# Kernel tuning notes

Measured on AMD Instinct MI355X. Metric: run time of the kernel, lower is better.

The kernel has to match this reference:

```python
import jax, jax.numpy as jnp
import numpy as np

B, N1, R12, R23 = 1, 4096, 4, 4
N2, N3 = N1 * R12, N1 * R12 * R23
D, F, H, NCLS, K = 1024, 512, 256, 4, 256


def setup_inputs() -> dict:
    key = jax.random.key(0)
    ks = jax.random.split(key, 10)
    s = 0.02
    return {
        "x1": jax.random.normal(ks[0], (B, N1, D), jnp.float32),
        "x2": jax.random.normal(ks[1], (B, N2, D), jnp.float32),
        "x3": jax.random.normal(ks[2], (B, N3, D), jnp.float32),
        # 3 fc layers (low/mid/high mag): Linear(D->F)
        "fcW": (jax.random.normal(ks[3], (3, D, F), jnp.float32) * s),
        "fcb": jnp.zeros((3, F), jnp.float32),
        # 5 gated-attention modules: 0=ga_low,1=ga_mid,2=ga_high,3=aux_low,4=aux_mid
        "gaWa": (jax.random.normal(ks[4], (5, F, H), jnp.float32) * s),
        "gaba": jnp.zeros((5, H), jnp.float32),
        "gaWb": (jax.random.normal(ks[5], (5, F, H), jnp.float32) * s),
        "gabb": jnp.zeros((5, H), jnp.float32),
        "gaWc": (jax.random.normal(ks[6], (5, H, 1), jnp.float32) * s),
        "gabc": jnp.zeros((5, 1), jnp.float32),
        "Wh": (jax.random.normal(ks[7], (F, NCLS), jnp.float32) * s),
        "bh": jnp.zeros((NCLS,), jnp.float32),
        "k_sample": K,
    }


def _ga(x, i, Wa, ba, Wb, bb, Wc, bc):
    # GatedAttention: tanh branch * sigmoid branch -> Linear(H->1); returns (B,N)
    a = jnp.tanh(x @ Wa[i] + ba[i])
    g = jax.nn.sigmoid(x @ Wb[i] + bb[i])
    return ((a * g) @ Wc[i] + bc[i])[..., 0]


def _block_gather(x, idx, ratio):
    # Equivalent to einsum('bkn,bnd->bkd', kron(one_hot(idx), eye(ratio)), x):
    # pick contiguous blocks of `ratio` rows for each selected coarse index.
    b, n, d = x.shape
    xb = x.reshape(b, n // ratio, ratio, d)
    out = jnp.take_along_axis(xb, idx[:, :, None, None], axis=1)  # (B,k,ratio,D)
    return out.reshape(b, idx.shape[1] * ratio, d)


def reference(x1, x2, x3, fcW, fcb, gaWa, gaba, gaWb, gabb, gaWc, gabc, Wh, bh, k_sample):
    ga = (gaWa, gaba, gaWb, gabb, gaWc, gabc)
    n1, n2, n3 = x1.shape[1], x2.shape[1], x3.shape[1]

    # --- low mag ---
    h1 = jax.nn.relu(x1 @ fcW[0] + fcb[0])                    # (B,N1,F)
    A1 = jax.nn.softmax(_ga(h1, 0, *ga), axis=-1)             # (B,N1)
    M1 = jnp.einsum('bn,bnf->bf', A1, h1)                     # (B,F)
    A1_aux = jax.nn.softmax(_ga(h1, 3, *ga), axis=-1)
    k1 = min(n1, int(k_sample))
    idx1 = jnp.sort(jax.lax.top_k(A1_aux, k1)[1], axis=-1)    # (B,k1)

    # zoom: gather selected blocks from mid and high mag features
    x2s = _block_gather(x2, idx1, n2 // n1)                   # (B,k1*R12,D)
    x3s = _block_gather(x3, idx1, n3 // n1)                   # (B,k1*R12*R23,D)

    # --- mid mag ---
    h2 = jax.nn.relu(x2s @ fcW[1] + fcb[1])
    A2 = jax.nn.softmax(_ga(h2, 1, *ga), axis=-1)
    M2 = jnp.einsum('bn,bnf->bf', A2, h2)
    A2_aux = jax.nn.softmax(_ga(h2, 4, *ga), axis=-1)
    k2 = min(h2.shape[1], int(k_sample))
    idx2 = jnp.sort(jax.lax.top_k(A2_aux, k2)[1], axis=-1)

    x3s2 = _block_gather(x3s, idx2, n3 // n2)                 # (B,k2*R23,D)

    # --- high mag ---
    h3 = jax.nn.relu(x3s2 @ fcW[2] + fcb[2])
    A3 = jax.nn.softmax(_ga(h3, 2, *ga), axis=-1)
    M3 = jnp.einsum('bn,bnf->bf', A3, h3)

    M = M1 + M2 + M3                                           # (B,F)
    logits = M @ Wh + bh                                       # (B,NCLS)
    return logits
```

## Files before the change

kernel.cpp:

```cpp
#include <hip/hip_runtime.h>
#include <hip/hip_bf16.h>
#include <math.h>


typedef __attribute__((ext_vector_type(8))) short short8;
typedef __attribute__((ext_vector_type(4))) float float4a;

__device__ __forceinline__ ushort f2bf(float f) {
    unsigned u = __float_as_uint(f);
    return (ushort)((u + 0x7fffu + ((u >> 16) & 1u)) >> 16);
}
__device__ __forceinline__ uint pk2(float a, float b) {
    __hip_bfloat162 t = __float22bfloat162_rn(make_float2(a, b));
    uint u; __builtin_memcpy(&u, &t, 4); return u;
}
__device__ __forceinline__ float aload(const float* p) {
    return __hip_atomic_load(p, __ATOMIC_RELAXED, __HIP_MEMORY_SCOPE_AGENT);
}

template<int SPLIT>
__global__ __launch_bounds__(256) void zm_hgemm(
    const float* __restrict__ A, int lda,
    const int* __restrict__ rowmap,
    const ushort* __restrict__ Bt,
    const float* __restrict__ bias,
    float* __restrict__ Cf, ushort* __restrict__ Cb, int ldc, int K)
{
    __shared__ ushort As[64 * 40];
    __shared__ ushort Bs[64 * 40];
    const int tid = threadIdx.x;
    const int brow = blockIdx.y << 6;
    const int bcol = blockIdx.x << 6;
    const int kbeg = SPLIT ? ((int)blockIdx.z << 8) : 0;
    const int kend = SPLIT ? kbeg + 256 : K;

    const int sr = tid >> 2;
    const int sk = (tid & 3) << 3;
    int arow = brow + sr;
    if (rowmap) arow = rowmap[arow];
    const float* Ap = A + (size_t)arow * lda;
    const ushort* Bp = Bt + (size_t)(bcol + sr) * K + sk;

    const int w = tid >> 6;
    const int wm = (w >> 1) << 5;
    const int wn = (w & 1) << 5;
    const int lane = tid & 63;
    const int lm = lane & 15;
    const int lq = lane >> 4;

    float4a acc[2][2] = {};

    for (int k0 = kbeg; k0 < kend; k0 += 32) {
        const float* ap = Ap + k0 + sk;
        float4 v0 = *(const float4*)(ap);
        float4 v1 = *(const float4*)(ap + 4);
        uint4 p0;
        p0.x = pk2(v0.x, v0.y); p0.y = pk2(v0.z, v0.w);
        p0.z = pk2(v1.x, v1.y); p0.w = pk2(v1.z, v1.w);
        *(uint4*)&As[sr * 40 + sk] = p0;
        *(uint4*)&Bs[sr * 40 + sk] = *(const uint4*)(Bp + k0);
        __syncthreads();
        short8 afr[2], bfr[2];
#pragma unroll
        for (int mt = 0; mt < 2; mt++)
            afr[mt] = *(const short8*)&As[(wm + mt * 16 + lm) * 40 + lq * 8];
#pragma unroll
        for (int nt = 0; nt < 2; nt++)
            bfr[nt] = *(const short8*)&Bs[(wn + nt * 16 + lm) * 40 + lq * 8];
#pragma unroll
        for (int mt = 0; mt < 2; mt++)
#pragma unroll
            for (int nt = 0; nt < 2; nt++)
                acc[mt][nt] = __builtin_amdgcn_mfma_f32_16x16x32_bf16(
                    afr[mt], bfr[nt], acc[mt][nt], 0, 0, 0);
        __syncthreads();
    }

#pragma unroll
    for (int mt = 0; mt < 2; mt++) {
#pragma unroll
        for (int nt = 0; nt < 2; nt++) {
            int gc = bcol + wn + nt * 16 + lm;
            float bv = bias[gc];
            if (SPLIT && blockIdx.z != 0) bv = 0.0f;
#pragma unroll
            for (int r = 0; r < 4; r++) {
                int gr = brow + wm + mt * 16 + lq * 4 + r;
                float v = acc[mt][nt][r] + bv;
                if (SPLIT) {
                    atomicAdd(&Cf[(size_t)gr * ldc + gc], v);
                } else {
                    v = fmaxf(v, 0.0f);
                    Cf[(size_t)gr * ldc + gc] = v;
                    Cb[(size_t)gr * ldc + gc] = f2bf(v);
                }
            }
        }
    }
}

template<int AMODE>
__global__ __launch_bounds__(256) void zm_sgemm(
    const void* __restrict__ Av, int lda,
    const ushort* __restrict__ Bt,
    const float* __restrict__ bint,
    const float* __restrict__ wc0, const float* __restrict__ wc1,
    float* __restrict__ sMain, float* __restrict__ sAux,
    float* __restrict__ statsOut, int* __restrict__ cnt2, int lastBlk)
{
    __shared__ ushort As[64 * 40];
    __shared__ ushort Bs[64 * 40];
    __shared__ float part[4][64];
    const int tid = threadIdx.x;
    const int brow = blockIdx.y << 6;
    const int bcol = blockIdx.x << 6;

    const int sr = tid >> 2;
    const int sk = (tid & 3) << 3;
    const float*  Af = (const float*)Av;
    const ushort* Ab = (const ushort*)Av;
    const ushort* Bp = Bt + (size_t)(bcol + sr) * 512 + sk;

    const int w = tid >> 6;
    const int wn = w << 4;
    const int lane = tid & 63;
    const int lm = lane & 15;
    const int lq = lane >> 4;

    float4a acc[4] = {};

    for (int k0 = 0; k0 < 512; k0 += 32) {
        if (AMODE == 0) {
            *(uint4*)&As[sr * 40 + sk] =
                *(const uint4*)(Ab + (size_t)(brow + sr) * lda + k0 + sk);
        } else {
            const float* ap = Af + (size_t)(brow + sr) * lda + k0 + sk;
            float4 v0 = *(const float4*)ap;
            float4 v1 = *(const float4*)(ap + 4);
            v0.x = fmaxf(v0.x, 0.f); v0.y = fmaxf(v0.y, 0.f);
            v0.z = fmaxf(v0.z, 0.f); v0.w = fmaxf(v0.w, 0.f);
            v1.x = fmaxf(v1.x, 0.f); v1.y = fmaxf(v1.y, 0.f);
            v1.z = fmaxf(v1.z, 0.f); v1.w = fmaxf(v1.w, 0.f);
            uint4 pk;
            pk.x = pk2(v0.x, v0.y); pk.y = pk2(v0.z, v0.w);
            pk.z = pk2(v1.x, v1.y); pk.w = pk2(v1.z, v1.w);
            *(uint4*)&As[sr * 40 + sk] = pk;
        }
        *(uint4*)&Bs[sr * 40 + sk] = *(const uint4*)(Bp + k0);
        __syncthreads();
        short8 bfr = *(const short8*)&Bs[(wn + lm) * 40 + lq * 8];
#pragma unroll
        for (int mt = 0; mt < 4; mt++) {
            short8 afr = *(const short8*)&As[(mt * 16 + lm) * 40 + lq * 8];
            acc[mt] = __builtin_amdgcn_mfma_f32_16x16x32_bf16(afr, bfr, acc[mt], 0, 0, 0);
        }
        __syncthreads();
    }

    const int gc = bcol + wn + lm;
    const float* wcp = (gc >= 512) ? wc1 : wc0;
    const float wcv = wcp[(gc & 511) >> 1];
    const float bv = bint[gc];
    const bool odd = (gc & 1);
    float* sp = (bcol >= 512) ? sAux : sMain;

#pragma unroll
    for (int mt = 0; mt < 4; mt++) {
        float red[4];
#pragma unroll
        for (int r = 0; r < 4; r++) {
            float v = acc[mt][r] + bv;
            float x = odd ? (1.0f / (1.0f + expf(-v))) : tanhf(v);
            float prt = __shfl_xor(x, 1);
            float ctr = odd ? 0.0f : (x * prt * wcv);
            ctr += __shfl_xor(ctr, 1);
            ctr += __shfl_xor(ctr, 2);
            ctr += __shfl_xor(ctr, 4);
            ctr += __shfl_xor(ctr, 8);
            red[r] = ctr;
        }
        if (lm == 0) {
#pragma unroll
            for (int r = 0; r < 4; r++) part[w][mt * 16 + lq * 4 + r] = red[r];
        }
    }
    __syncthreads();
    if (tid < 64) {
        float tot = part[0][tid] + part[1][tid] + part[2][tid] + part[3][tid];
        atomicAdd(&sp[brow + tid], tot);
    }

    if (statsOut) {
        __threadfence();
        __shared__ int lastf;
        if (tid == 0)
            lastf = (__hip_atomic_fetch_add(cnt2, 1, __ATOMIC_ACQ_REL,
                                            __HIP_MEMORY_SCOPE_AGENT) == lastBlk);
        __syncthreads();
        if (lastf) {
            float* red = (float*)part;
            float vv[4];
            float mx = -3.4e38f;
#pragma unroll
            for (int j = 0; j < 4; j++) {
                vv[j] = aload(&sMain[tid + j * 256]);
                mx = fmaxf(mx, vv[j]);
            }
            red[tid] = mx; __syncthreads();
            for (int o = 128; o > 0; o >>= 1) {
                if (tid < o) red[tid] = fmaxf(red[tid], red[tid + o]);
                __syncthreads();
            }
            mx = red[0]; __syncthreads();
            float z = 0.0f;
#pragma unroll
            for (int j = 0; j < 4; j++) z += expf(vv[j] - mx);
            red[tid] = z; __syncthreads();
            for (int o = 128; o > 0; o >>= 1) {
                if (tid < o) red[tid] += red[tid + o];
                __syncthreads();
            }
            if (tid == 0) { statsOut[0] = mx; statsOut[1] = red[0]; }
        }
    }
}

__global__ __launch_bounds__(1024) void zm_topk(
    const float* __restrict__ sa, const float* __restrict__ sm, int n,
    const int* __restrict__ idx_prev,
    int* __restrict__ idx_out, int* __restrict__ rm_out,
    float* __restrict__ stOut)
{
    __shared__ float redf[1024];
    __shared__ int hist[256];
    __shared__ int idxbuf[256];
    __shared__ int wsum[16];
    __shared__ int bcastB, bcastAbove;
    const int bs = 1024;
    const int tid = threadIdx.x;

    if (blockIdx.x == 1) {
        float mx = -3.4e38f;
        for (int i = tid; i < n; i += bs) mx = fmaxf(mx, sm[i]);
        redf[tid] = mx; __syncthreads();
        for (int o = 512; o > 0; o >>= 1) {
            if (tid < o) redf[tid] = fmaxf(redf[tid], redf[tid + o]);
            __syncthreads();
        }
        mx = redf[0]; __syncthreads();
        float z = 0.0f;
        for (int i = tid; i < n; i += bs) z += expf(sm[i] - mx);
        redf[tid] = z; __syncthreads();
        for (int o = 512; o > 0; o >>= 1) {
            if (tid < o) redf[tid] += redf[tid + o];
            __syncthreads();
        }
        if (tid == 0) { stOut[0] = mx; stOut[1] = redf[0]; }
        return;
    }

    const int ept = n >> 10;
    const int lane = tid & 63;
    unsigned key[4];
#pragma unroll
    for (int e = 0; e < 4; e++) key[e] = 0;
    for (int e = 0; e < ept; e++) {
        unsigned u = __float_as_uint(sa[tid * ept + e]);
        key[e] = (u & 0x80000000u) ? ~u : (u | 0x80000000u);
    }

    unsigned prefix = 0;
    int remaining = 256;
    for (int pass = 0; pass < 4; pass++) {
        const int shift = 24 - pass * 8;
        if (tid < 256) hist[tid] = 0;
        __syncthreads();
        for (int e = 0; e < ept; e++) {
            unsigned k = key[e];
            bool ok = (pass == 0) || ((k >> (shift + 8)) == (prefix >> (shift + 8)));
            if (ok) atomicAdd(&hist[(k >> shift) & 0xff], 1);
        }
        __syncthreads();
        if (tid < 64) {
            int h0 = hist[lane * 4 + 0], h1 = hist[lane * 4 + 1];
            int h2 = hist[lane * 4 + 2], h3 = hist[lane * 4 + 3];
            int q = h0 + h1 + h2 + h3;
            int suf = q;
#pragma unroll
            for (int o = 1; o < 64; o <<= 1) {
                int v = __shfl_down(suf, o);
                if (lane + o < 64) suf += v;
            }
            int above = suf - q;
            int c3 = above + h3;
            int c2 = c3 + h2;
            int c1 = c2 + h1;
            int c0 = c1 + h0;
            int cc[4]  = {c0, c1, c2, c3};
            int nxt[4] = {c1, c2, c3, above};
#pragma unroll
            for (int j = 0; j < 4; j++)
                if (cc[j] >= remaining && nxt[j] < remaining) {
                    bcastB = lane * 4 + j;
                    bcastAbove = nxt[j];
                }
        }
        __syncthreads();
        prefix |= ((unsigned)bcastB) << shift;
        remaining -= bcastAbove;
        __syncthreads();
    }
    const unsigned T = prefix;
    const int m = remaining;

    int gt = 0, eq = 0;
    for (int e = 0; e < ept; e++) { gt += (key[e] > T); eq += (key[e] == T); }
    int packed = (gt << 16) | eq;
    int incl = packed;
#pragma unroll
    for (int o = 1; o < 64; o <<= 1) {
        int v = __shfl_up(incl, o);
        if (lane >= o) incl += v;
    }
    if (lane == 63) wsum[tid >> 6] = incl;
    __syncthreads();
    if (tid < 64) {
        int v = (tid < 16) ? wsum[tid] : 0;
        int s = v;
#pragma unroll
        for (int o = 1; o < 16; o <<= 1) {
            int t2 = __shfl_up(s, o);
            if (tid >= o) s += t2;
        }
        if (tid < 16) wsum[tid] = s - v;
    }
    __syncthreads();
    int base = wsum[tid >> 6] + incl - packed;
    int gt_before = base >> 16;
    int eq_before = base & 0xffff;
    for (int e = 0; e < ept; e++) {
        if (key[e] > T) {
            int eqa = (eq_before < m) ? eq_before : m;
            idxbuf[gt_before + eqa] = tid * ept + e;
            gt_before++;
        } else if (key[e] == T) {
            if (eq_before < m) idxbuf[gt_before + eq_before] = tid * ept + e;
            eq_before++;
        }
    }
    __syncthreads();
    if (tid < 256) idx_out[tid] = idxbuf[tid];
    int t = idxbuf[tid >> 2] * 4 + (tid & 3);
    rm_out[tid] = idx_prev ? (idx_prev[t >> 4] * 16 + (t & 15)) : t;
}

__global__ __launch_bounds__(256) void zm_prep(
    const float* __restrict__ fcW,
    const float* __restrict__ gaWa, const float* __restrict__ gaWb,
    const float* __restrict__ gaba, const float* __restrict__ gabb,
    ushort* __restrict__ fc_t, ushort* __restrict__ gint,
    float* __restrict__ bint, float4* __restrict__ zbase, int zn4)
{
    const int b = blockIdx.x;
    const int tid = threadIdx.x;
    if (b >= 2817) {
        float4 z4 = make_float4(0.f, 0.f, 0.f, 0.f);
        for (int i = (b - 2817) * 256 + tid; i < zn4; i += 64 * 256)
            zbase[i] = z4;
        return;
    }
    if (b == 2816) {
        for (int i = tid; i < 2560; i += 256) {
            int n, head;
            if (i < 1024)      { n = i;        head = (n >> 9) ? 3 : 0; }
            else if (i < 2048) { n = i - 1024; head = (n >> 9) ? 4 : 1; }
            else               { n = i - 2048; head = 2; }
            int h = (n & 511) >> 1;
            const float* src = (n & 1) ? gabb : gaba;
            bint[i] = src[head * 256 + h];
        }
        return;
    }
    __shared__ ushort tile[32][33];
    const int c = tid & 31, r8 = tid >> 5;
    if (b < 1536) {
        int mat = b >> 9, rem = b & 511;
        int tk = rem >> 4, tn = rem & 15;
        const float* src = fcW + (size_t)mat * 1024 * 512;
        ushort* dst = fc_t + (size_t)mat * 512 * 1024;
        int k0 = tk * 32, n0 = tn * 32;
#pragma unroll
        for (int it = 0; it < 4; it++) {
            int r = r8 + it * 8;
            tile[r][c] = f2bf(src[(size_t)(k0 + r) * 512 + n0 + c]);
        }
        __syncthreads();
#pragma unroll
        for (int it = 0; it < 4; it++) {
            int r = r8 + it * 8;
            dst[(size_t)(n0 + r) * 1024 + k0 + c] = tile[c][r];
        }
    } else {
        int idx = b - 1536;
        int mat = idx >> 7, rem = idx & 127;
        int tk = rem >> 3, th = rem & 7;
        int head = mat >> 1, br = mat & 1;
        const float* src = (br ? gaWb : gaWa) + (size_t)head * 512 * 256;
        ushort* dstb; int off;
        if (head == 0)      { dstb = gint;              off = 0;   }
        else if (head == 1) { dstb = gint + 1024 * 512; off = 0;   }
        else if (head == 2) { dstb = gint + 2048 * 512; off = 0;   }
        else if (head == 3) { dstb = gint;              off = 512; }
        else                { dstb = gint + 1024 * 512; off = 512; }
        int k0 = tk * 32, h0 = th * 32;
#pragma unroll
        for (int it = 0; it < 4; it++) {
            int r = r8 + it * 8;
            tile[r][c] = f2bf(src[(size_t)(k0 + r) * 256 + h0 + c]);
        }
        __syncthreads();
#pragma unroll
        for (int it = 0; it < 4; it++) {
            int r = r8 + it * 8;
            dstb[(size_t)(off + 2 * (h0 + r) + br) * 512 + k0 + c] = tile[c][r];
        }
    }
}

__global__ __launch_bounds__(256) void zm_final(
    const float* __restrict__ h1f, const float* __restrict__ h2f,
    const float* __restrict__ h3f,
    const float* __restrict__ s1, const float* __restrict__ s2,
    const float* __restrict__ s3,
    const float* __restrict__ st, float* __restrict__ Mbuf,
    int* __restrict__ cnt,
    const float* __restrict__ Wh, const float* __restrict__ bh,
    float* __restrict__ out)
{
    const int tid = threadIdx.x;
    const int b = blockIdx.x;
    const float* h; const float* s; const float* stp; int r0, rl;
    if (b < 64)      { h = h1f; s = s1; stp = st;     r0 = b * 64;        rl = 0; }
    else if (b < 80) { h = h2f; s = s2; stp = st + 2; r0 = (b - 64) * 64; rl = 1; }
    else             { h = h3f; s = s3; stp = st + 4; r0 = (b - 80) * 64; rl = 1; }
    const float mx = stp[0];
    const float invZ = 1.0f / stp[1];
    float a0 = 0.0f, a1 = 0.0f;
    for (int r = 0; r < 64; r++) {
        int n = r0 + r;
        float wgt = expf(s[n] - mx) * invZ;
        float v0 = h[(size_t)n * 512 + tid];
        float v1 = h[(size_t)n * 512 + 256 + tid];
        if (rl) { v0 = fmaxf(v0, 0.f); v1 = fmaxf(v1, 0.f); }
        a0 += wgt * v0; a1 += wgt * v1;
    }
    atomicAdd(&Mbuf[tid], a0);
    atomicAdd(&Mbuf[tid + 256], a1);
    __threadfence();
    __shared__ int lastf;
    if (tid == 0)
        lastf = (__hip_atomic_fetch_add(cnt, 1, __ATOMIC_ACQ_REL,
                                        __HIP_MEMORY_SCOPE_AGENT) == 95);
    __syncthreads();
    if (lastf) {
        const int c = tid >> 6, lane = tid & 63;
        float pacc = 0.0f;
        for (int f = lane; f < 512; f += 64)
            pacc += aload(&Mbuf[f]) * Wh[f * 4 + c];
        for (int o = 32; o > 0; o >>= 1) pacc += __shfl_down(pacc, o);
        if (lane == 0) out[c] = pacc + bh[c];
    }
}

extern "C" void kernel_launch(void* const* d_in, const int* in_sizes, int n_in,
                              void* d_out, int out_size, void* d_ws, size_t ws_size,
                              hipStream_t stream)
{
    const float* x1   = (const float*)d_in[0];
    const float* x2   = (const float*)d_in[1];
    const float* x3   = (const float*)d_in[2];
    const float* fcW  = (const float*)d_in[3];
    const float* fcb  = (const float*)d_in[4];
    const float* gaWa = (const float*)d_in[5];
    const float* gaba = (const float*)d_in[6];
    const float* gaWb = (const float*)d_in[7];
    const float* gabb = (const float*)d_in[8];
    const float* gaWc = (const float*)d_in[9];
    const float* Wh   = (const float*)d_in[11];
    const float* bh   = (const float*)d_in[12];
    float* out = (float*)d_out;

    char* p = (char*)d_ws;
    float*  h1f  = (float*)p;
    ushort* h1b  = (ushort*)(p + 8388608);
    ushort* fc_t = (ushort*)(p + 12582912);
    ushort* gint = (ushort*)(p + 15728640);
    float*  bint = (float*)(p + 18350080);
    float*  st   = (float*)(p + 18360320);
    int*    idx1 = (int*)(p + 18360352);
    int*    idx2 = (int*)(p + 18361376);
    int*    rm2  = (int*)(p + 18362400);
    int*    rm3  = (int*)(p + 18366496);
    char*   zbase = p + 18370592;
    float*  h2f  = (float*)zbase;
    float*  h3f  = (float*)(zbase + 2097152);
    float*  s1   = (float*)(zbase + 4194304);
    float*  s1a  = (float*)(zbase + 4210688);
    float*  s2   = (float*)(zbase + 4227072);
    float*  s2a  = (float*)(zbase + 4231168);
    float*  s3   = (float*)(zbase + 4235264);
    float*  Mbuf = (float*)(zbase + 4239360);
    int*    cnt  = (int*)(zbase + 4241408);
    const int ZN4 = 4241424 / 16;

    zm_prep<<<2881, 256, 0, stream>>>(fcW, gaWa, gaWb, gaba, gabb,
                                      fc_t, gint, bint, (float4*)zbase, ZN4);
    zm_hgemm<0><<<dim3(8, 64), 256, 0, stream>>>(x1, 1024, nullptr, fc_t, fcb,
                                                 h1f, h1b, 512, 1024);
    zm_sgemm<0><<<dim3(16, 64), 256, 0, stream>>>(h1b, 512, gint, bint,
                                                  gaWc, gaWc + 3 * 256,
                                                  s1, s1a, nullptr, nullptr, 0);
    zm_topk<<<2, 1024, 0, stream>>>(s1a, s1, 4096, nullptr, idx1, rm2, st);
    zm_hgemm<1><<<dim3(8, 16, 4), 256, 0, stream>>>(x2, 1024, rm2,
                                                    fc_t + 512 * 1024, fcb + 512,
                                                    h2f, nullptr, 512, 1024);
    zm_sgemm<1><<<dim3(16, 16), 256, 0, stream>>>(h2f, 512, gint + 1024 * 512,
                                                  bint + 1024,
                                                  gaWc + 256, gaWc + 4 * 256,
                                                  s2, s2a, nullptr, nullptr, 0);
    zm_topk<<<2, 1024, 0, stream>>>(s2a, s2, 1024, idx1, idx2, rm3, st + 2);
    zm_hgemm<1><<<dim3(8, 16, 4), 256, 0, stream>>>(x3, 1024, rm3,
                                                    fc_t + 2 * 512 * 1024, fcb + 1024,
                                                    h3f, nullptr, 512, 1024);
    zm_sgemm<1><<<dim3(8, 16), 256, 0, stream>>>(h3f, 512, gint + 2048 * 512,
                                                 bint + 2048,
                                                 gaWc + 2 * 256, gaWc + 2 * 256,
                                                 s3, s3, st + 4, cnt + 1, 127);
    zm_final<<<96, 256, 0, stream>>>(h1f, h2f, h3f, s1, s2, s3, st, Mbuf, cnt,
                                     Wh, bh, out);
}
```

Before: 528.1 us.

## Pre-convert x1 to bf16 in prep kernel and rewrite top-k radix select

The prep kernel gains extra blocks that convert x1 from fp32 to bf16 into a scratch buffer, so the first GEMM loads bf16 A tiles directly instead of converting inside the K loop, now selected through a new ABF template flag. The top-k kernel's 4-pass 8-bit radix select is replaced by 11-bit histogram levels over a compacted candidate list in shared memory, finishing with a brute-force rank among the remaining candidates. The aim is to cut per-tile conversion work and the number of select passes. In exchange it costs an extra write and read of x1 in bf16, a larger scratch footprint, and more shared memory in the top-k kernel.

```diff
diff --git a/kernel.cpp b/kernel.cpp
--- a/kernel.cpp
+++ b/kernel.cpp
@@ -18,9 +18,9 @@
     return __hip_atomic_load(p, __ATOMIC_RELAXED, __HIP_MEMORY_SCOPE_AGENT);
 }
 
-template<int SPLIT>
+template<int SPLIT, int ABF>
 __global__ __launch_bounds__(256) void zm_hgemm(
-    const float* __restrict__ A, int lda,
+    const void* __restrict__ Av, int lda,
     const int* __restrict__ rowmap,
     const ushort* __restrict__ Bt,
     const float* __restrict__ bias,
@@ -38,7 +38,8 @@
     const int sk = (tid & 3) << 3;
     int arow = brow + sr;
     if (rowmap) arow = rowmap[arow];
-    const float* Ap = A + (size_t)arow * lda;
+    const float*  Apf = (const float*)Av + (size_t)arow * lda;
+    const ushort* Apb = (const ushort*)Av + (size_t)arow * lda;
     const ushort* Bp = Bt + (size_t)(bcol + sr) * K + sk;
 
     const int w = tid >> 6;
@@ -51,13 +52,17 @@
     float4a acc[2][2] = {};
 
     for (int k0 = kbeg; k0 < kend; k0 += 32) {
-        const float* ap = Ap + k0 + sk;
-        float4 v0 = *(const float4*)(ap);
-        float4 v1 = *(const float4*)(ap + 4);
-        uint4 p0;
-        p0.x = pk2(v0.x, v0.y); p0.y = pk2(v0.z, v0.w);
-        p0.z = pk2(v1.x, v1.y); p0.w = pk2(v1.z, v1.w);
-        *(uint4*)&As[sr * 40 + sk] = p0;
+        if (ABF) {
+            *(uint4*)&As[sr * 40 + sk] = *(const uint4*)(Apb + k0 + sk);
+        } else {
+            const float* ap = Apf + k0 + sk;
+            float4 v0 = *(const float4*)(ap);
+            float4 v1 = *(const float4*)(ap + 4);
+            uint4 p0;
+            p0.x = pk2(v0.x, v0.y); p0.y = pk2(v0.z, v0.w);
+            p0.z = pk2(v1.x, v1.y); p0.w = pk2(v1.z, v1.w);
+            *(uint4*)&As[sr * 40 + sk] = p0;
+        }
         *(uint4*)&Bs[sr * 40 + sk] = *(const uint4*)(Bp + k0);
         __syncthreads();
         short8 afr[2], bfr[2];
@@ -232,10 +237,13 @@
     float* __restrict__ stOut)
 {
     __shared__ float redf[1024];
-    __shared__ int hist[256];
+    __shared__ int hist[2048];
+    __shared__ unsigned ckey[4096];
+    __shared__ int cidx[4096];
     __shared__ int idxbuf[256];
     __shared__ int wsum[16];
-    __shared__ int bcastB, bcastAbove;
+    __shared__ int bc[4];
+    __shared__ unsigned bcT;
     const int bs = 1024;
     const int tid = threadIdx.x;
 
@@ -269,49 +277,90 @@
         key[e] = (u & 0x80000000u) ? ~u : (u | 0x80000000u);
     }
 
-    unsigned prefix = 0;
-    int remaining = 256;
-    for (int pass = 0; pass < 4; pass++) {
-        const int shift = 24 - pass * 8;
-        if (tid < 256) hist[tid] = 0;
-        __syncthreads();
-        for (int e = 0; e < ept; e++) {
-            unsigned k = key[e];
-            bool ok = (pass == 0) || ((k >> (shift + 8)) == (prefix >> (shift + 8)));
-            if (ok) atomicAdd(&hist[(k >> shift) & 0xff], 1);
-        }
-        __syncthreads();
-        if (tid < 64) {
-            int h0 = hist[lane * 4 + 0], h1 = hist[lane * 4 + 1];
-            int h2 = hist[lane * 4 + 2], h3 = hist[lane * 4 + 3];
-            int q = h0 + h1 + h2 + h3;
-            int suf = q;
-#pragma unroll
-            for (int o = 1; o < 64; o <<= 1) {
-                int v = __shfl_down(suf, o);
-                if (lane + o < 64) suf += v;
+    int need = 256;
+    int c = 0;
+    for (int level = 0; level < 3; level++) {
+        const int shift = (level == 0) ? 21 : ((level == 1) ? 10 : 0);
+        hist[tid] = 0; hist[tid + 1024] = 0;
+        if (tid == 0) bc[2] = 0;
+        __syncthreads();
+        if (level == 0) {
+            for (int e = 0; e < ept; e++) atomicAdd(&hist[key[e] >> 21], 1);
+        } else {
+            for (int j = tid; j < c; j += bs)
+                atomicAdd(&hist[(ckey[j] >> shift) & 2047], 1);
+        }
+        __syncthreads();
+        int h0 = hist[2 * tid], h1 = hist[2 * tid + 1];
+        int q = h0 + h1;
+        int suf = q;
+#pragma unroll
+        for (int o = 1; o < 64; o <<= 1) {
+            int v = __shfl_down(suf, o);
+            if (lane + o < 64) suf += v;
+        }
+        if (lane == 0) wsum[tid >> 6] = suf;
+        __syncthreads();
+        if (tid < 16) {
+            int v = wsum[tid];
+            int s = v;
+#pragma unroll
+            for (int o = 1; o < 16; o <<= 1) {
+                int t2 = __shfl_down(s, o);
+                if (tid + o < 16) s += t2;
             }
-            int above = suf - q;
-            int c3 = above + h3;
-            int c2 = c3 + h2;
-            int c1 = c2 + h1;
-            int c0 = c1 + h0;
-            int cc[4]  = {c0, c1, c2, c3};
-            int nxt[4] = {c1, c2, c3, above};
-#pragma unroll
-            for (int j = 0; j < 4; j++)
-                if (cc[j] >= remaining && nxt[j] < remaining) {
-                    bcastB = lane * 4 + j;
-                    bcastAbove = nxt[j];
+            wsum[tid] = s - v;
+        }
+        __syncthreads();
+        int abv1 = wsum[tid >> 6] + (suf - q);
+        int abv0 = abv1 + h1;
+        if (abv1 < need && abv1 + h1 >= need) { bc[0] = 2 * tid + 1; bc[1] = abv1; }
+        if (abv0 < need && abv0 + h0 >= need) { bc[0] = 2 * tid;     bc[1] = abv0; }
+        __syncthreads();
+        const int B = bc[0];
+        const int above = bc[1];
+        if (level == 0) {
+            for (int e = 0; e < ept; e++)
+                if ((int)(key[e] >> 21) == B) {
+                    int s2 = atomicAdd(&bc[2], 1);
+                    ckey[s2] = key[e]; cidx[s2] = tid * ept + e;
                 }
-        }
-        __syncthreads();
-        prefix |= ((unsigned)bcastB) << shift;
-        remaining -= bcastAbove;
-        __syncthreads();
-    }
-    const unsigned T = prefix;
-    const int m = remaining;
+            __syncthreads();
+        } else {
+            unsigned rk[4]; int ri[4]; int rc = 0;
+            for (int j = tid; j < c; j += bs)
+                if ((int)((ckey[j] >> shift) & 2047) == B) {
+                    rk[rc] = ckey[j]; ri[rc] = cidx[j]; rc++;
+                }
+            __syncthreads();
+            for (int qq = 0; qq < rc; qq++) {
+                int s2 = atomicAdd(&bc[2], 1);
+                ckey[s2] = rk[qq]; cidx[s2] = ri[qq];
+            }
+            __syncthreads();
+        }
+        c = bc[2];
+        need -= above;
+        if (c <= 256 || level == 2) break;
+    }
+
+    if (tid == 0) bc[3] = 0;
+    __syncthreads();
+    for (int j = tid; j < c; j += bs) {
+        unsigned kj = ckey[j]; int ij = cidx[j];
+        int rank = 0;
+        for (int i = 0; i < c; i++) {
+            unsigned ki = ckey[i];
+            rank += (ki > kj) || (ki == kj && cidx[i] < ij);
+        }
+        if (rank == need - 1) bcT = kj;
+    }
+    __syncthreads();
+    const unsigned T = bcT;
+    for (int j = tid; j < c; j += bs)
+        if (ckey[j] > T) atomicAdd(&bc[3], 1);
+    __syncthreads();
+    const int m = need - bc[3];
 
     int gt = 0, eq = 0;
     for (int e = 0; e < ept; e++) { gt += (key[e] > T); eq += (key[e] == T); }
@@ -359,10 +408,24 @@
     const float* __restrict__ gaWa, const float* __restrict__ gaWb,
     const float* __restrict__ gaba, const float* __restrict__ gabb,
     ushort* __restrict__ fc_t, ushort* __restrict__ gint,
-    float* __restrict__ bint, float4* __restrict__ zbase, int zn4)
+    float* __restrict__ bint, float4* __restrict__ zbase, int zn4,
+    const float* __restrict__ x1, ushort* __restrict__ x1b)
 {
     const int b = blockIdx.x;
     const int tid = threadIdx.x;
+    if (b >= 2881) {
+        const int base = ((b - 2881) * 256 + tid) * 8;
+        for (int it = 0; it < 8; it++) {
+            int i = base + it * 524288;
+            float4 a = *(const float4*)(x1 + i);
+            float4 b4 = *(const float4*)(x1 + i + 4);
+            uint4 o;
+            o.x = pk2(a.x, a.y); o.y = pk2(a.z, a.w);
+            o.z = pk2(b4.x, b4.y); o.w = pk2(b4.z, b4.w);
+            *(uint4*)(x1b + i) = o;
+        }
+        return;
+    }
     if (b >= 2817) {
         float4 z4 = make_float4(0.f, 0.f, 0.f, 0.f);
         for (int i = (b - 2817) * 256 + tid; i < zn4; i += 64 * 256)
@@ -512,26 +575,30 @@
     float*  Mbuf = (float*)(zbase + 4239360);
     int*    cnt  = (int*)(zbase + 4241408);
     const int ZN4 = 4241424 / 16;
-
-    zm_prep<<<2881, 256, 0, stream>>>(fcW, gaWa, gaWb, gaba, gabb,
-                                      fc_t, gint, bint, (float4*)zbase, ZN4);
-    zm_hgemm<0><<<dim3(8, 64), 256, 0, stream>>>(x1, 1024, nullptr, fc_t, fcb,
-                                                 h1f, h1b, 512, 1024);
+    ushort* x1b  = (ushort*)(p + 22612032);
+
+    zm_prep<<<3137, 256, 0, stream>>>(fcW, gaWa, gaWb, gaba, gabb,
+                                      fc_t, gint, bint, (float4*)zbase, ZN4,
+                                      x1, x1b);
+    zm_hgemm<0, 1><<<dim3(8, 64), 256, 0, stream>>>(x1b, 1024, nullptr, fc_t,
+                                                    fcb, h1f, h1b, 512, 1024);
     zm_sgemm<0><<<dim3(16, 64), 256, 0, stream>>>(h1b, 512, gint, bint,
                                                   gaWc, gaWc + 3 * 256,
                                                   s1, s1a, nullptr, nullptr, 0);
     zm_topk<<<2, 1024, 0, stream>>>(s1a, s1, 4096, nullptr, idx1, rm2, st);
-    zm_hgemm<1><<<dim3(8, 16, 4), 256, 0, stream>>>(x2, 1024, rm2,
-                                                    fc_t + 512 * 1024, fcb + 512,
-                                                    h2f, nullptr, 512, 1024);
+    zm_hgemm<1, 0><<<dim3(8, 16, 4), 256, 0, stream>>>(x2, 1024, rm2,
+                                                       fc_t + 512 * 1024,
+                                                       fcb + 512,
+                                                       h2f, nullptr, 512, 1024);
     zm_sgemm<1><<<dim3(16, 16), 256, 0, stream>>>(h2f, 512, gint + 1024 * 512,
                                                   bint + 1024,
                                                   gaWc + 256, gaWc + 4 * 256,
                                                   s2, s2a, nullptr, nullptr, 0);
     zm_topk<<<2, 1024, 0, stream>>>(s2a, s2, 1024, idx1, idx2, rm3, st + 2);
-    zm_hgemm<1><<<dim3(8, 16, 4), 256, 0, stream>>>(x3, 1024, rm3,
-                                                    fc_t + 2 * 512 * 1024, fcb + 1024,
-                                                    h3f, nullptr, 512, 1024);
+    zm_hgemm<1, 0><<<dim3(8, 16, 4), 256, 0, stream>>>(x3, 1024, rm3,
+                                                       fc_t + 2 * 512 * 1024,
+                                                       fcb + 1024,
+                                                       h3f, nullptr, 512, 1024);
     zm_sgemm<1><<<dim3(8, 16), 256, 0, stream>>>(h3f, 512, gint + 2048 * 512,
                                                  bint + 2048,
                                                  gaWc + 2 * 256, gaWc + 2 * 256,
```

Measured after the change: 527.0 us. About the same (-0.2%).
